# Kernel tuning notes

Hardware: AMD Instinct MI355X
Metric: run time of the kernel (lower is better)

The kernel has to match this reference:

```python
import jax, jax.numpy as jnp
import numpy as np


def setup_inputs() -> dict:
    key = jax.random.key(0)
    kx, kw = jax.random.split(key)
    x = jax.random.normal(kx, (32, 128, 8192), dtype=jnp.float32)
    weight = jax.random.normal(kw, (128, 128, 1, 2), dtype=jnp.float32)
    return {"x": x, "weight": weight}


def reference(x, weight):
    # x: (bs, cin, d); weight: (cout, cin, 1, 2)
    bs, cin, d = x.shape
    xp = x.reshape(bs, cin, d // 2, 2)          # (bs, cin, d/2, 2)
    w = weight[:, :, 0, :]                      # (cout, cin, 2)
    # out[b, o, p] = sum_{c,k} x[b,c,p,k] * w[o,c,k] / sqrt(cin)
    out = jnp.einsum('bcpk,ock->bop', xp, w) / jnp.sqrt(jnp.float32(cin))
    return out
```

## Files before the change

### kernel.cpp

```cpp
#include <hip/hip_runtime.h>
#include <stdint.h>


typedef __attribute__((ext_vector_type(8))) short bf16x8;
typedef __attribute__((ext_vector_type(4))) float f32x4;

#define CIN  128
#define DLEN 8192
#define PLEN 4096
#define COUT 128

__device__ inline unsigned short f2bf(float f) {
    unsigned u = __builtin_bit_cast(unsigned, f);
    unsigned r = u + 0x7FFFu + ((u >> 16) & 1u);
    return (unsigned short)(r >> 16);
}

__device__ inline unsigned pack_bf(float a, float b) {
    unsigned ua = __builtin_bit_cast(unsigned, a);
    unsigned ub = __builtin_bit_cast(unsigned, b);
    unsigned ra = ua + 0x7FFFu + ((ua >> 16) & 1u);
    unsigned rb = ub + 0x7FFFu + ((ub >> 16) & 1u);
    return (ra >> 16) | (rb & 0xFFFF0000u);
}

__global__ __launch_bounds__(256) void convert_w(const float* __restrict__ w,
                                                 unsigned short* __restrict__ wb) {
    int t  = blockIdx.x * 256 + threadIdx.x;
    int o  = t >> 7;
    int k0 = (t & 127) * 2;
    const float scale = 0.088388347648318447f;
    float2 f = *(const float2*)(w + o * 256 + k0);
    unsigned v = (unsigned)f2bf(f.x * scale) | ((unsigned)f2bf(f.y * scale) << 16);
    int idx = (k0 >> 3) * 1024 + o * 8 + (k0 & 7);
    *(unsigned*)(wb + idx) = v;
}

__global__ __launch_bounds__(256, 4) void conv_mfma(const float* __restrict__ x,
                                                    const unsigned short* __restrict__ wb,
                                                    float* __restrict__ out) {
    int tile = blockIdx.x;
    int b    = tile >> 5;
    int pt   = (tile & 31) * 128;
    int lane = threadIdx.x & 63;
    int w    = threadIdx.x >> 6;
    int quad = lane >> 4;
    int l16  = lane & 15;
    int pbase = pt + w * 32;

    const float* xl = x + (size_t)b * ((size_t)CIN * DLEN)
                        + (size_t)(quad * 4) * DLEN + 2 * pbase + 4 * l16;
    const uint32_t* bb = (const uint32_t*)wb + quad * 512 + l16 * 4;

    f32x4 acc[2][8];
#pragma unroll
    for (int mt = 0; mt < 2; ++mt)
#pragma unroll
        for (int t = 0; t < 8; ++t)
            acc[mt][t] = (f32x4)(0.0f);

    float4 abuf[4];
#pragma unroll
    for (int jj = 0; jj < 4; ++jj)
        abuf[jj] = *(const float4*)(xl + (size_t)jj * DLEN);

#pragma unroll 1
    for (int kc = 0; kc < 8; ++kc) {
        union { bf16x8 v; unsigned uu[4]; } afr0, afr1;
#pragma unroll
        for (int jj = 0; jj < 4; ++jj) {
            afr0.uu[jj] = pack_bf(abuf[jj].x, abuf[jj].y);
            afr1.uu[jj] = pack_bf(abuf[jj].z, abuf[jj].w);
        }
        if (kc < 7) {
            const float* nx = xl + (size_t)((kc + 1) * 16) * DLEN;
#pragma unroll
            for (int jj = 0; jj < 4; ++jj)
                abuf[jj] = *(const float4*)(nx + (size_t)jj * DLEN);
        }
        const uint32_t* bk = bb + kc * 2048;
#pragma unroll
        for (int th = 0; th < 2; ++th) {
            union { bf16x8 v; uint4 u; } bfr[4];
#pragma unroll
            for (int tt = 0; tt < 4; ++tt)
                bfr[tt].u = *(const uint4*)(bk + (th * 4 + tt) * 64);
#pragma unroll
            for (int tt = 0; tt < 4; ++tt) {
                int t = th * 4 + tt;
                acc[0][t] = __builtin_amdgcn_mfma_f32_16x16x32_bf16(afr0.v, bfr[tt].v, acc[0][t], 0, 0, 0);
                acc[1][t] = __builtin_amdgcn_mfma_f32_16x16x32_bf16(afr1.v, bfr[tt].v, acc[1][t], 0, 0, 0);
            }
        }
    }

    float* ob = out + (size_t)b * ((size_t)COUT * PLEN) + pbase + quad * 8;
#pragma unroll
    for (int t = 0; t < 8; ++t) {
        int o = t * 16 + l16;
        float* orow = ob + (size_t)o * PLEN;
        f32x4 v0 = { acc[0][t][0], acc[1][t][0], acc[0][t][1], acc[1][t][1] };
        f32x4 v1 = { acc[0][t][2], acc[1][t][2], acc[0][t][3], acc[1][t][3] };
        *(f32x4*)(orow)     = v0;
        *(f32x4*)(orow + 4) = v1;
    }
}

extern "C" void kernel_launch(void* const* d_in, const int* in_sizes, int n_in,
                              void* d_out, int out_size, void* d_ws, size_t ws_size,
                              hipStream_t stream) {
    const float* x = (const float*)d_in[0];
    const float* w = (const float*)d_in[1];
    float* out = (float*)d_out;
    unsigned short* wb = (unsigned short*)d_ws;

    convert_w<<<64, 256, 0, stream>>>(w, wb);
    conv_mfma<<<1024, 256, 0, stream>>>(x, wb, out);
}
```

Baseline: 212.7 us.

## Fuse weight conversion into conv kernel via LDS staging and deepen x prefetch

Removes the separate weight-conversion kernel; each block loads the fp32 weights, scales and packs them to bf16 into 64KB of shared memory, then reads B fragments from LDS. The x loads are double-buffered two K-chunks ahead and the K loop is fully unrolled, with launch bounds lowered to 2 blocks per SM. This saves a kernel launch and global B reads but redoes the weight conversion in every block and limits occupancy via LDS usage.

```diff
diff --git a/kernel.cpp b/kernel.cpp
--- a/kernel.cpp
+++ b/kernel.cpp
@@ -10,12 +10,6 @@
 #define PLEN 4096
 #define COUT 128
 
-__device__ inline unsigned short f2bf(float f) {
-    unsigned u = __builtin_bit_cast(unsigned, f);
-    unsigned r = u + 0x7FFFu + ((u >> 16) & 1u);
-    return (unsigned short)(r >> 16);
-}
-
 __device__ inline unsigned pack_bf(float a, float b) {
     unsigned ua = __builtin_bit_cast(unsigned, a);
     unsigned ub = __builtin_bit_cast(unsigned, b);
@@ -24,33 +18,40 @@
     return (ra >> 16) | (rb & 0xFFFF0000u);
 }
 
-__global__ __launch_bounds__(256) void convert_w(const float* __restrict__ w,
-                                                 unsigned short* __restrict__ wb) {
-    int t  = blockIdx.x * 256 + threadIdx.x;
-    int o  = t >> 7;
-    int k0 = (t & 127) * 2;
-    const float scale = 0.088388347648318447f;
-    float2 f = *(const float2*)(w + o * 256 + k0);
-    unsigned v = (unsigned)f2bf(f.x * scale) | ((unsigned)f2bf(f.y * scale) << 16);
-    int idx = (k0 >> 3) * 1024 + o * 8 + (k0 & 7);
-    *(unsigned*)(wb + idx) = v;
-}
+__global__ __launch_bounds__(256, 2) void conv_mfma(const float* __restrict__ x,
+                                                    const float* __restrict__ w,
+                                                    float* __restrict__ out) {
+    __shared__ uint4 bsh4[4096];
+    int tid = threadIdx.x;
 
-__global__ __launch_bounds__(256, 4) void conv_mfma(const float* __restrict__ x,
-                                                    const unsigned short* __restrict__ wb,
-                                                    float* __restrict__ out) {
+    {
+        const float4* w4 = (const float4*)w;
+        uint2* bsh2 = (uint2*)bsh4;
+        int o2 = tid >> 1, half = tid & 1;
+        const float s = 0.088388347648318447f;
+#pragma unroll
+        for (int j = 0; j < 32; ++j) {
+            float4 f = w4[o2 * 64 + j * 2 + half];
+            uint2 v;
+            v.x = pack_bf(f.x * s, f.y * s);
+            v.y = pack_bf(f.z * s, f.w * s);
+            bsh2[j * 256 + tid] = v;
+        }
+    }
+    __syncthreads();
+    const uint32_t* bsh = (const uint32_t*)bsh4;
+
     int tile = blockIdx.x;
     int b    = tile >> 5;
     int pt   = (tile & 31) * 128;
-    int lane = threadIdx.x & 63;
-    int w    = threadIdx.x >> 6;
+    int lane = tid & 63;
+    int wv   = tid >> 6;
     int quad = lane >> 4;
     int l16  = lane & 15;
-    int pbase = pt + w * 32;
+    int pbase = pt + wv * 32;
 
     const float* xl = x + (size_t)b * ((size_t)CIN * DLEN)
                         + (size_t)(quad * 4) * DLEN + 2 * pbase + 4 * l16;
-    const uint32_t* bb = (const uint32_t*)wb + quad * 512 + l16 * 4;
 
     f32x4 acc[2][8];
 #pragma unroll
@@ -59,38 +60,36 @@
         for (int t = 0; t < 8; ++t)
             acc[mt][t] = (f32x4)(0.0f);
 
-    float4 abuf[4];
+    float4 abuf[2][4];
 #pragma unroll
     for (int jj = 0; jj < 4; ++jj)
-        abuf[jj] = *(const float4*)(xl + (size_t)jj * DLEN);
+        abuf[0][jj] = *(const float4*)(xl + (size_t)jj * DLEN);
+#pragma unroll
+    for (int jj = 0; jj < 4; ++jj)
+        abuf[1][jj] = *(const float4*)(xl + (size_t)(16 + jj) * DLEN);
 
-#pragma unroll 1
+#pragma unroll
     for (int kc = 0; kc < 8; ++kc) {
         union { bf16x8 v; unsigned uu[4]; } afr0, afr1;
 #pragma unroll
         for (int jj = 0; jj < 4; ++jj) {
-            afr0.uu[jj] = pack_bf(abuf[jj].x, abuf[jj].y);
-            afr1.uu[jj] = pack_bf(abuf[jj].z, abuf[jj].w);
+            float4 v = abuf[kc & 1][jj];
+            afr0.uu[jj] = pack_bf(v.x, v.y);
+            afr1.uu[jj] = pack_bf(v.z, v.w);
         }
-        if (kc < 7) {
-            const float* nx = xl + (size_t)((kc + 1) * 16) * DLEN;
+        if (kc < 6) {
+            const float* nx = xl + (size_t)((kc + 2) * 16) * DLEN;
 #pragma unroll
             for (int jj = 0; jj < 4; ++jj)
-                abuf[jj] = *(const float4*)(nx + (size_t)jj * DLEN);
+                abuf[kc & 1][jj] = *(const float4*)(nx + (size_t)jj * DLEN);
         }
-        const uint32_t* bk = bb + kc * 2048;
+        const uint32_t* bk = bsh + (kc * 4 + quad) * 512 + l16 * 4;
 #pragma unroll
-        for (int th = 0; th < 2; ++th) {
-            union { bf16x8 v; uint4 u; } bfr[4];
-#pragma unroll
-            for (int tt = 0; tt < 4; ++tt)
-                bfr[tt].u = *(const uint4*)(bk + (th * 4 + tt) * 64);
-#pragma unroll
-            for (int tt = 0; tt < 4; ++tt) {
-                int t = th * 4 + tt;
-                acc[0][t] = __builtin_amdgcn_mfma_f32_16x16x32_bf16(afr0.v, bfr[tt].v, acc[0][t], 0, 0, 0);
-                acc[1][t] = __builtin_amdgcn_mfma_f32_16x16x32_bf16(afr1.v, bfr[tt].v, acc[1][t], 0, 0, 0);
-            }
+        for (int t = 0; t < 8; ++t) {
+            union { bf16x8 v; uint4 u; } bfr;
+            bfr.u = *(const uint4*)(bk + t * 64);
+            acc[0][t] = __builtin_amdgcn_mfma_f32_16x16x32_bf16(afr0.v, bfr.v, acc[0][t], 0, 0, 0);
+            acc[1][t] = __builtin_amdgcn_mfma_f32_16x16x32_bf16(afr1.v, bfr.v, acc[1][t], 0, 0, 0);
         }
     }
 
@@ -112,8 +111,7 @@
     const float* x = (const float*)d_in[0];
     const float* w = (const float*)d_in[1];
     float* out = (float*)d_out;
-    unsigned short* wb = (unsigned short*)d_ws;
+    (void)d_ws; (void)ws_size;
 
-    convert_w<<<64, 256, 0, stream>>>(w, wb);
-    conv_mfma<<<1024, 256, 0, stream>>>(x, wb, out);
+    conv_mfma<<<1024, 256, 0, stream>>>(x, w, out);
 }
```

New measurement: 220.5 us. 1.04x slower.
